# Kernel tuning notes

Hardware: AMD Instinct MI355X
Metric: run time of the kernel (lower is better)

The kernel has to match this reference:

```python
import jax, jax.numpy as jnp
import numpy as np

N = 8192
D = 256
E = 262144


def setup_inputs() -> dict:
    key = jax.random.key(0)
    kx, ke = jax.random.split(key)
    x = jax.random.normal(kx, (N, D), dtype=jnp.float32)
    edge_index = jax.random.randint(ke, (2, E), 0, N, dtype=jnp.int64)
    return {"x": x, "edge_index": edge_index}


def reference(x, edge_index):
    n, d = x.shape
    xs = x / (d ** 0.25)
    # per-edge similarity: equivalent to einsum('md,nd->mn')[src, dst] without O(n^2 d)
    src, dst = edge_index[0], edge_index[1]
    vals = jnp.einsum('ed,ed->e', xs[src], xs[dst])
    neg = jnp.finfo(jnp.float32).min
    sim = jnp.full((n, n), neg, dtype=x.dtype)
    sim = sim.at[src, dst].set(vals)
    # logaritmic=False branch: plain double softmax, averaged
    scores0 = jax.nn.softmax(sim, axis=1)                # row softmax
    scores1 = jax.nn.softmax(sim, axis=0)                # col softmax (== softmax(sim.T, -1).T)
    scores = (scores0 + scores1) * 0.5
    return scores, sim
```

## Files before the change

### kernel.cpp

```cpp
#include <hip/hip_runtime.h>
#include <float.h>
#include <math.h>

constexpr int Nn = 8192;
constexpr unsigned BG = 0xFF7F0000u;

typedef unsigned u32x4 __attribute__((ext_vector_type(4)));

__device__ __forceinline__ float clamp01(float f) {
    return fminf(fmaxf(f, 0.0f), 1.0f);
}

__device__ __forceinline__ void load_edge(const unsigned* ew, unsigned F, int E, int e,
                                          int& s, int& d) {
    s = (int)(ew[e << F] & (Nn - 1));
    d = (int)(ew[(E << F) + (e << F)] & (Nn - 1));
}

__device__ __forceinline__ float stat_ss(float sr) {
    return sr + (sr == 0.0f ? (float)Nn : 0.0f);
}
__device__ __forceinline__ float stat_bgp(float sr) {
    return (sr == 0.0f) ? (1.0f / (float)Nn) : 0.0f;
}

__global__ void k1_fill(u32x4* __restrict__ sim4, const unsigned* __restrict__ ew,
                        unsigned* __restrict__ flag, float* __restrict__ rowsum,
                        float* __restrict__ colsum) {
    int tid = blockIdx.x * 256 + threadIdx.x;
    u32x4 bg = {BG, BG, BG, BG};
    sim4[2 * tid] = bg;
    sim4[2 * tid + 1] = bg;
    if (tid < Nn) {
        rowsum[tid] = 0.0f;
        colsum[tid] = 0.0f;
    }
    if (blockIdx.x == 0) {
        __shared__ unsigned acc;
        if (threadIdx.x == 0) acc = 0u;
        __syncthreads();
        atomicOr(&acc, ew[2 * threadIdx.x + 1]);
        __syncthreads();
        if (threadIdx.x == 0) flag[0] = (acc == 0u) ? 1u : 0u;
    }
}

__global__ void k2_edges(const float* __restrict__ x, const unsigned* __restrict__ ew,
                         const unsigned* __restrict__ flag, unsigned* __restrict__ sim_u,
                         float* __restrict__ vals,
                         float* __restrict__ rowsum, float* __restrict__ colsum, int E) {
    int lane = threadIdx.x & 63;
    int wid = threadIdx.x >> 6;
    int g = lane >> 4;
    int t = lane & 15;
    int e = (blockIdx.x * 4 + wid) * 4 + g;
    if (e >= E) return;
    unsigned F = flag[0];
    int s, d;
    load_edge(ew, F, E, e, s, d);
    const float4* xa = (const float4*)x + (((size_t)s) << 6);
    const float4* xb = (const float4*)x + (((size_t)d) << 6);
    float v = 0.0f;
    #pragma unroll
    for (int i = 0; i < 4; ++i) {
        float4 a = xa[t + 16 * i];
        float4 b = xb[t + 16 * i];
        v += a.x * b.x + a.y * b.y + a.z * b.z + a.w * b.w;
    }
    #pragma unroll
    for (int off = 8; off; off >>= 1) v += __shfl_xor(v, off);
    v *= 0.0625f;
    if (t == 0) {
        vals[e] = v;
        unsigned cell = (unsigned)s * (unsigned)Nn + (unsigned)d;
        unsigned old = atomicExch(&sim_u[cell], __float_as_uint(v));
        if (old == BG) {
            float ev = expf(v);
            atomicAdd(&rowsum[s], ev);
            atomicAdd(&colsum[d], ev);
        }
    }
}

__global__ void k3_out(const unsigned* __restrict__ ew, const unsigned* __restrict__ flag,
                       const float* __restrict__ vals,
                       const float* __restrict__ rowsum, const float* __restrict__ colsum,
                       float* __restrict__ scores, int E, int EB) {
    int b = blockIdx.x;
    if (b < EB) {
        int e = b * 256 + threadIdx.x;
        if (e >= E) return;
        unsigned F = flag[0];
        int s, d;
        load_edge(ew, F, E, e, s, d);
        float hr = 0.5f / stat_ss(rowsum[s]);
        float hc = 0.5f / stat_ss(colsum[d]);
        float sc = clamp01(expf(vals[e]) * (hr + hc));
        scores[(size_t)s * Nn + d] = sc;
        return;
    }
    int r = b - EB;
    if (r < Nn) {
        float ri = stat_bgp(rowsum[r]);
        if (ri == 0.0f) return;
        for (int j = threadIdx.x; j < Nn; j += 256)
            scores[(size_t)r * Nn + j] = clamp01(0.5f * (ri + stat_bgp(colsum[j])));
    } else {
        int j = r - Nn;
        float cj = stat_bgp(colsum[j]);
        if (cj == 0.0f) return;
        for (int i = threadIdx.x; i < Nn; i += 256)
            scores[(size_t)i * Nn + j] = clamp01(0.5f * (stat_bgp(rowsum[i]) + cj));
    }
}

extern "C" void kernel_launch(void* const* d_in, const int* in_sizes, int n_in,
                              void* d_out, int out_size, void* d_ws, size_t ws_size,
                              hipStream_t stream) {
    const float* x = (const float*)d_in[0];
    const unsigned* ew = (const unsigned*)d_in[1];
    const int E = in_sizes[1] / 2;

    float* scores = (float*)d_out;
    float* sim = scores + (size_t)Nn * (size_t)Nn;

    char* w = (char*)d_ws;
    unsigned* flag = (unsigned*)w;  w += 16;
    float* vals = (float*)w;        w += (size_t)E * 4;
    float* rowsum = (float*)w;      w += (size_t)Nn * 4;
    float* colsum = (float*)w;      w += (size_t)Nn * 4;

    const int EB = (E + 255) / 256;
    k1_fill<<<(Nn / 8) * Nn / 256, 256, 0, stream>>>((u32x4*)sim, ew, flag, rowsum, colsum);
    k2_edges<<<(E + 15) / 16, 256, 0, stream>>>(x, ew, flag, (unsigned*)sim, vals,
                                                rowsum, colsum, E);
    k3_out<<<EB + 2 * Nn, 256, 0, stream>>>(ew, flag, vals, rowsum, colsum, scores, E, EB);
}
```

Measured before the change: 570.5 us.

## Overlap sim background fill with edge dot products and dedup via hash table

The dense background fill of sim is merged into the edge kernel by interleaving blocks, two fill blocks for every edge block, so the bulk memory writes overlap with the gather and dot-product work. Because sim is no longer guaranteed to be filled before an edge is written, first-occurrence detection moves from atomicExch on sim to a separate 1M-entry open-addressing hash with atomicCAS. The per-edge sim values are now written in the output kernel. This adds a 4MB hash init plus probe loops, and it relies on duplicate edges producing identical values.

```diff
diff --git a/kernel.cpp b/kernel.cpp
--- a/kernel.cpp
+++ b/kernel.cpp
@@ -4,6 +4,8 @@
 
 constexpr int Nn = 8192;
 constexpr unsigned BG = 0xFF7F0000u;
+constexpr unsigned EMPTY = 0xFFFFFFFFu;
+constexpr unsigned HSZ = 1u << 20;
 
 typedef unsigned u32x4 __attribute__((ext_vector_type(4)));
 
@@ -24,13 +26,11 @@
     return (sr == 0.0f) ? (1.0f / (float)Nn) : 0.0f;
 }
 
-__global__ void k1_fill(u32x4* __restrict__ sim4, const unsigned* __restrict__ ew,
-                        unsigned* __restrict__ flag, float* __restrict__ rowsum,
-                        float* __restrict__ colsum) {
+__global__ void k0_init(unsigned* __restrict__ hash, float* __restrict__ rowsum,
+                        float* __restrict__ colsum, const unsigned* __restrict__ ew,
+                        unsigned* __restrict__ flag) {
     int tid = blockIdx.x * 256 + threadIdx.x;
-    u32x4 bg = {BG, BG, BG, BG};
-    sim4[2 * tid] = bg;
-    sim4[2 * tid + 1] = bg;
+    hash[tid] = EMPTY;
     if (tid < Nn) {
         rowsum[tid] = 0.0f;
         colsum[tid] = 0.0f;
@@ -45,15 +45,26 @@
     }
 }
 
-__global__ void k2_edges(const float* __restrict__ x, const unsigned* __restrict__ ew,
-                         const unsigned* __restrict__ flag, unsigned* __restrict__ sim_u,
-                         float* __restrict__ vals,
-                         float* __restrict__ rowsum, float* __restrict__ colsum, int E) {
+__global__ void k1_main(u32x4* __restrict__ sim4, const float* __restrict__ x,
+                        const unsigned* __restrict__ ew, const unsigned* __restrict__ flag,
+                        unsigned* __restrict__ hash, float* __restrict__ vals,
+                        float* __restrict__ rowsum, float* __restrict__ colsum, int E) {
+    int b = blockIdx.x;
+    int m = b % 3;
+    if (m != 2) {
+        int fb = (b / 3) * 2 + m;
+        int tid = fb * 256 + threadIdx.x;
+        u32x4 bg = {BG, BG, BG, BG};
+        sim4[2 * tid] = bg;
+        sim4[2 * tid + 1] = bg;
+        return;
+    }
+    int eb = b / 3;
     int lane = threadIdx.x & 63;
     int wid = threadIdx.x >> 6;
     int g = lane >> 4;
     int t = lane & 15;
-    int e = (blockIdx.x * 4 + wid) * 4 + g;
+    int e = (eb * 4 + wid) * 4 + g;
     if (e >= E) return;
     unsigned F = flag[0];
     int s, d;
@@ -64,17 +75,24 @@
     #pragma unroll
     for (int i = 0; i < 4; ++i) {
         float4 a = xa[t + 16 * i];
-        float4 b = xb[t + 16 * i];
-        v += a.x * b.x + a.y * b.y + a.z * b.z + a.w * b.w;
+        float4 bb = xb[t + 16 * i];
+        v += a.x * bb.x + a.y * bb.y + a.z * bb.z + a.w * bb.w;
     }
     #pragma unroll
     for (int off = 8; off; off >>= 1) v += __shfl_xor(v, off);
     v *= 0.0625f;
     if (t == 0) {
         vals[e] = v;
-        unsigned cell = (unsigned)s * (unsigned)Nn + (unsigned)d;
-        unsigned old = atomicExch(&sim_u[cell], __float_as_uint(v));
-        if (old == BG) {
+        unsigned key = ((unsigned)s << 13) | (unsigned)d;
+        unsigned h = (key * 2654435761u) & (HSZ - 1);
+        bool own = false;
+        while (true) {
+            unsigned prev = atomicCAS(&hash[h], EMPTY, key);
+            if (prev == EMPTY) { own = true; break; }
+            if (prev == key) break;
+            h = (h + 1) & (HSZ - 1);
+        }
+        if (own) {
             float ev = expf(v);
             atomicAdd(&rowsum[s], ev);
             atomicAdd(&colsum[d], ev);
@@ -82,10 +100,10 @@
     }
 }
 
-__global__ void k3_out(const unsigned* __restrict__ ew, const unsigned* __restrict__ flag,
+__global__ void k2_out(const unsigned* __restrict__ ew, const unsigned* __restrict__ flag,
                        const float* __restrict__ vals,
                        const float* __restrict__ rowsum, const float* __restrict__ colsum,
-                       float* __restrict__ scores, int E, int EB) {
+                       float* __restrict__ scores, float* __restrict__ sim, int E, int EB) {
     int b = blockIdx.x;
     if (b < EB) {
         int e = b * 256 + threadIdx.x;
@@ -93,10 +111,12 @@
         unsigned F = flag[0];
         int s, d;
         load_edge(ew, F, E, e, s, d);
+        float v = vals[e];
+        size_t cell = (size_t)s * Nn + d;
         float hr = 0.5f / stat_ss(rowsum[s]);
         float hc = 0.5f / stat_ss(colsum[d]);
-        float sc = clamp01(expf(vals[e]) * (hr + hc));
-        scores[(size_t)s * Nn + d] = sc;
+        scores[cell] = clamp01(expf(v) * (hr + hc));
+        sim[cell] = v;
         return;
     }
     int r = b - EB;
@@ -127,12 +147,14 @@
     char* w = (char*)d_ws;
     unsigned* flag = (unsigned*)w;  w += 16;
     float* vals = (float*)w;        w += (size_t)E * 4;
+    unsigned* hash = (unsigned*)w;  w += (size_t)HSZ * 4;
     float* rowsum = (float*)w;      w += (size_t)Nn * 4;
     float* colsum = (float*)w;      w += (size_t)Nn * 4;
 
     const int EB = (E + 255) / 256;
-    k1_fill<<<(Nn / 8) * Nn / 256, 256, 0, stream>>>((u32x4*)sim, ew, flag, rowsum, colsum);
-    k2_edges<<<(E + 15) / 16, 256, 0, stream>>>(x, ew, flag, (unsigned*)sim, vals,
-                                                rowsum, colsum, E);
-    k3_out<<<EB + 2 * Nn, 256, 0, stream>>>(ew, flag, vals, rowsum, colsum, scores, E, EB);
+    k0_init<<<HSZ / 256, 256, 0, stream>>>(hash, rowsum, colsum, ew, flag);
+    k1_main<<<49152, 256, 0, stream>>>((u32x4*)sim, x, ew, flag, hash, vals,
+                                       rowsum, colsum, E);
+    k2_out<<<EB + 2 * Nn, 256, 0, stream>>>(ew, flag, vals, rowsum, colsum,
+                                            scores, sim, E, EB);
 }
```

Result: slower. 596.4 us (+4.5%).
